# Kernel optimization log

Measured on AMD Instinct MI355X. Metric: run time of the kernel, lower is better.

## Reference

```python
import jax, jax.numpy as jnp
import numpy as np

B, L, H, E = 8, 4096, 8, 64  # in_channels = out_channels = H*E = 512
MODES = 64                   # mode_select_method='else' -> indices = range(MODES)
SCALE = 1.0 / (512 * 512)


def setup_inputs() -> dict:
    key = jax.random.key(0)
    kq, kk, kv, k1, k2 = jax.random.split(key, 5)
    q = jax.random.normal(kq, (B, L, H, E), dtype=jnp.float32)
    k = jax.random.normal(kk, (B, L, H, E), dtype=jnp.float32)
    v = jax.random.normal(kv, (B, L, H, E), dtype=jnp.float32)
    # weights: [num_heads, in_ch//heads, out_ch//heads, modes], scaled randn
    w1 = SCALE * jax.random.normal(k1, (H, E, E, MODES), dtype=jnp.float32)
    w2 = SCALE * jax.random.normal(k2, (H, E, E, MODES), dtype=jnp.float32)
    return {"q": q, "k": k, "v": v, "w1": w1, "w2": w2}


def reference(q, k, v, w1, w2):
    # k, v, mask are unused by FourierBlock.forward
    Bq, Lq, Hq, Eq = q.shape
    modes = w1.shape[-1]
    x = jnp.transpose(q, (0, 2, 3, 1))          # [B, H, E, L]
    x_ft = jnp.fft.rfft(x, axis=-1)             # [B, H, E, L//2+1] complex
    # With mode_select_method='else', selected indices are 0..modes-1.
    W = (w1 + 1j * w2).astype(x_ft.dtype)       # [H, E_in, E_out, modes]
    # Fused gather + batched complex matmul over all modes (replaces the per-mode loop)
    out_ft = jnp.einsum('bhim,hiom->bhom', x_ft[..., :modes], W)  # [B, H, E, modes]
    # irfft with n=L zero-pads the freq axis from `modes` up to L//2+1 (FEDformer quirk)
    x_out = jnp.fft.irfft(out_ft, n=Lq, axis=-1)  # [B, H, E, L] real
    return jnp.transpose(x_out, (0, 3, 1, 2))     # [B, L, H, E]
```

## Files before the change

### kernel.cpp

```cpp
#include <hip/hip_runtime.h>
#include <hip/hip_bf16.h>
#include <math.h>

#define NB 8
#define LN 4096
#define NH 8
#define NE 64
#define NC 512
#define NM 64
#define LMASK 4095

typedef short s16x8 __attribute__((ext_vector_type(8)));
typedef float f32x4 __attribute__((ext_vector_type(4)));
typedef const __attribute__((address_space(1))) void gv_t;
typedef __attribute__((address_space(3))) void lv_t;

#define WS_EGF 0
#define WS_TF  262144
#define WS_GF  524288
#define WS_XP  786432
#define WS_XS  4980736

static __device__ __forceinline__ unsigned short bf16bits(float f) {
    __hip_bfloat16 b = __float2bfloat16(f);
    return *reinterpret_cast<unsigned short*>(&b);
}

__global__ __launch_bounds__(256) void k_tables(unsigned short* __restrict__ egf,
                                                unsigned short* __restrict__ tfp) {
    const int bid = blockIdx.x;
    const int s = (bid & 255) * 256 + threadIdx.x;
    const int lane = s & 63;
    unsigned short v[8];
    if (bid < 256) {
        int mt = (s >> 6) & 7, kc = s >> 9;
        int r = lane & 15, kg = lane >> 4;
        int mpm = mt * 16 + r;
        int m = mpm >> 1, isim = mpm & 1;
        #pragma unroll
        for (int j = 0; j < 8; ++j) {
            int l = kc * 32 + kg * 8 + j;
            int tw = (m * l) & LMASK;
            float ang = (6.283185307179586f / 4096.0f) * (float)tw;
            v[j] = bf16bits(isim ? -sinf(ang) : cosf(ang));
        }
    } else {
        int lt = (s >> 6) & 255, kk = s >> 14;
        int l = lt * 16 + (lane & 15);
        int khi = (lane >> 4) * 8;
        #pragma unroll
        for (int j = 0; j < 8; ++j) {
            int mp = kk * 32 + khi + j;
            int m = mp >> 1;
            int tw = (m * l) & LMASK;
            float ang = (6.283185307179586f / 4096.0f) * (float)tw;
            v[j] = bf16bits((mp & 1) ? sinf(ang) : cosf(ang));
        }
    }
    uint4 pk;
    pk.x = (unsigned)v[0] | ((unsigned)v[1] << 16);
    pk.y = (unsigned)v[2] | ((unsigned)v[3] << 16);
    pk.z = (unsigned)v[4] | ((unsigned)v[5] << 16);
    pk.w = (unsigned)v[6] | ((unsigned)v[7] << 16);
    unsigned short* dst = (bid < 256) ? egf : tfp;
    *reinterpret_cast<uint4*>(dst + (size_t)s * 8) = pk;
}

__global__ __launch_bounds__(256, 2) void k_fs1(const float* __restrict__ q,
                                                const unsigned short* __restrict__ egf,
                                                float* __restrict__ xp) {
    __shared__ float qlds[4][4][32][16];
    __shared__ unsigned short eglds[4][4096];
    const int ks = blockIdx.x, h = blockIdx.y, b = blockIdx.z;
    const int tid = threadIdx.x;
    const int w = tid >> 6, lane = tid & 63;
    const int g = lane >> 4, r = lane & 15;

    const float* qsrc = q + (((size_t)b * LN + ks * 512 + (lane >> 2)) * NH + h) * NE
                          + w * 16 + (lane & 3) * 4;
    const unsigned short* esrc = egf + (size_t)(ks * 16) * 4096 + w * 1024 + lane * 8;

#define STAGE_Q(T) { \
    __builtin_amdgcn_global_load_lds((gv_t*)(qsrc + (size_t)(T) * 32 * NC), \
        (lv_t*)(&qlds[(T) & 3][w][0][0]), 16, 0, 0); \
    __builtin_amdgcn_global_load_lds((gv_t*)(qsrc + ((size_t)(T) * 32 + 16) * NC), \
        (lv_t*)(&qlds[(T) & 3][w][16][0]), 16, 0, 0); }

#define STAGE_E(T) { \
    __builtin_amdgcn_global_load_lds((gv_t*)(esrc + (size_t)(T) * 4096), \
        (lv_t*)(&eglds[(T) & 3][w * 1024]), 16, 0, 0); \
    __builtin_amdgcn_global_load_lds((gv_t*)(esrc + (size_t)(T) * 4096 + 512), \
        (lv_t*)(&eglds[(T) & 3][w * 1024 + 512]), 16, 0, 0); }

    f32x4 acc[8];
    #pragma unroll
    for (int mt = 0; mt < 8; ++mt) acc[mt] = (f32x4)(0.0f);

    STAGE_Q(0) STAGE_E(0) STAGE_E(1) STAGE_Q(1) STAGE_Q(2)

    #pragma unroll
    for (int t = 0; t < 16; ++t) {
        if (t + 2 < 16) STAGE_E(t + 2)
        if (t <= 13)      asm volatile("s_waitcnt vmcnt(8)" ::: "memory");
        else if (t == 14) asm volatile("s_waitcnt vmcnt(4)" ::: "memory");
        else              asm volatile("s_waitcnt vmcnt(0)" ::: "memory");
        __builtin_amdgcn_s_barrier();
        asm volatile("" ::: "memory");
        if (t + 3 < 16) STAGE_Q(t + 3)

        s16x8 af[8];
        #pragma unroll
        for (int mt = 0; mt < 8; ++mt)
            af[mt] = *reinterpret_cast<const s16x8*>(&eglds[t & 3][mt * 512 + lane * 8]);
        s16x8 bfr;
        #pragma unroll
        for (int j = 0; j < 8; ++j)
            bfr[j] = (short)bf16bits(qlds[t & 3][w][g * 8 + j][r]);

        #pragma unroll
        for (int mt = 0; mt < 8; ++mt)
            acc[mt] = __builtin_amdgcn_mfma_f32_16x16x32_bf16(af[mt], bfr, acc[mt], 0, 0, 0);
    }
#undef STAGE_Q
#undef STAGE_E

    const int i = w * 16 + r;
    float* xpb = xp + ((size_t)ks * 64 + b * 8 + h) * (64 * 128) + (size_t)i * 128 + g * 4;
    #pragma unroll
    for (int mt = 0; mt < 8; ++mt)
        *reinterpret_cast<f32x4*>(xpb + mt * 16) = acc[mt];
}

__global__ __launch_bounds__(256) void k_presum(const float* __restrict__ xp,
                                                float* __restrict__ xs) {
    int e4 = blockIdx.x * 256 + threadIdx.x;
    const f32x4* xp4 = reinterpret_cast<const f32x4*>(xp);
    f32x4 s = (f32x4)(0.0f);
    #pragma unroll
    for (int ks = 0; ks < 8; ++ks)
        s += __builtin_nontemporal_load(&xp4[(size_t)ks * 131072 + e4]);
    reinterpret_cast<f32x4*>(xs)[e4] = s;
}

__global__ __launch_bounds__(256) void k_s2(const float* __restrict__ w1,
                                            const float* __restrict__ w2,
                                            const float* __restrict__ xs,
                                            unsigned short* __restrict__ gf) {
    __shared__ float2 sxs[2][64][64];
    const int sid = blockIdx.x;
    const int x   = sid & 7;
    const int idx = sid >> 3;
    const int r   = x * 8 + (idx & 7);
    const int og  = r >> 3, h = r & 7;
    const int bb  = idx >> 3;
    const int tt  = threadIdx.x;

    {
        float4* dst = reinterpret_cast<float4*>(&sxs[0][0][0]);
        #pragma unroll
        for (int bs = 0; bs < 2; ++bs) {
            const float4* s4 = reinterpret_cast<const float4*>(
                xs + ((size_t)((bb * 2 + bs) * 8 + h)) * 8192);
            #pragma unroll
            for (int k = 0; k < 8; ++k)
                dst[bs * 2048 + k * 256 + tt] = s4[k * 256 + tt];
        }
    }
    __syncthreads();

    const int m    = tt & 63;
    const int osub = tt >> 6;
    const int o0   = og * 8 + osub * 2;

    float re[2][2], im[2][2];
    #pragma unroll
    for (int oo = 0; oo < 2; ++oo)
        #pragma unroll
        for (int bs = 0; bs < 2; ++bs) { re[oo][bs] = 0.f; im[oo][bs] = 0.f; }

    const float* w1p = w1 + (size_t)h * (NE * NE * NM) + (size_t)o0 * NM + m;
    const float* w2p = w2 + (size_t)h * (NE * NE * NM) + (size_t)o0 * NM + m;

    #pragma unroll 8
    for (int i = 0; i < NE; ++i) {
        float wr0 = w1p[(size_t)i * (NE * NM)];
        float wi0 = w2p[(size_t)i * (NE * NM)];
        float wr1 = w1p[(size_t)i * (NE * NM) + NM];
        float wi1 = w2p[(size_t)i * (NE * NM) + NM];
        #pragma unroll
        for (int bs = 0; bs < 2; ++bs) {
            float2 xv = sxs[bs][i][m];
            re[0][bs] = fmaf(xv.x, wr0, fmaf(-xv.y, wi0, re[0][bs]));
            im[0][bs] = fmaf(xv.x, wi0, fmaf( xv.y, wr0, im[0][bs]));
            re[1][bs] = fmaf(xv.x, wr1, fmaf(-xv.y, wi1, re[1][bs]));
            im[1][bs] = fmaf(xv.x, wi1, fmaf( xv.y, wr1, im[1][bs]));
        }
    }

    const float sca = (m == 0 ? 1.0f : 2.0f) / (float)LN;
    const int kk  = m >> 4;
    const int khi = ((m & 15) >> 2) * 16;
    const int jj  = (m & 3) << 1;
    #pragma unroll
    for (int oo = 0; oo < 2; ++oo) {
        const int c = h * 64 + o0 + oo;
        #pragma unroll
        for (int bs = 0; bs < 2; ++bs) {
            const int b = bb * 2 + bs;
            size_t slot = (((size_t)b * 4 + kk) * 32 + (c >> 4)) * 64 + khi + (c & 15);
            unsigned int pk = (unsigned)bf16bits(re[oo][bs] * sca) |
                              ((unsigned)bf16bits(-im[oo][bs] * sca) << 16);
            *reinterpret_cast<unsigned int*>(gf + slot * 8 + jj) = pk;
        }
    }
}

__global__ __launch_bounds__(256, 2) void k_s3(const unsigned short* __restrict__ gf,
                                               const unsigned short* __restrict__ tfp,
                                               float* __restrict__ out) {
    const int lb = blockIdx.x;
    const int cb = blockIdx.y;
    const int b  = blockIdx.z;
    const int tid = threadIdx.x;
    const int w = tid >> 6, lane = tid & 63;

    const unsigned short* ga = gf + ((((size_t)b * 4) * 32 + cb * 8 + w * 2) * 64 + lane) * 8;
    const unsigned short* tb = tfp + (((size_t)lb * 4) * 64 + lane) * 8;

    f32x4 acc[2][4] = {};
    s16x8 af[3][2], bf[3][4];

#define S3_LOAD(T, SLOT)                                                          \
    {                                                                             \
        const unsigned short* gp_ = ga + (size_t)(T) * (32 * 64 * 8);             \
        const unsigned short* tp_ = tb + (size_t)(T) * (256 * 64 * 8);            \
        af[SLOT][0] = *reinterpret_cast<const s16x8*>(gp_);                       \
        af[SLOT][1] = *reinterpret_cast<const s16x8*>(gp_ + 64 * 8);              \
        bf[SLOT][0] = *reinterpret_cast<const s16x8*>(tp_);                       \
        bf[SLOT][1] = *reinterpret_cast<const s16x8*>(tp_ + 64 * 8);              \
        bf[SLOT][2] = *reinterpret_cast<const s16x8*>(tp_ + 2 * 64 * 8);          \
        bf[SLOT][3] = *reinterpret_cast<const s16x8*>(tp_ + 3 * 64 * 8);          \
    }

    S3_LOAD(0, 0)
    S3_LOAD(1, 1)

    #pragma unroll
    for (int t = 0; t < 4; ++t) {
        const int slot = t % 3;
        if (t + 2 < 4) { const int ns = (t + 2) % 3; S3_LOAD(t + 2, ns) }
        #pragma unroll
        for (int mi = 0; mi < 2; ++mi)
            #pragma unroll
            for (int ni = 0; ni < 4; ++ni)
                acc[mi][ni] = __builtin_amdgcn_mfma_f32_16x16x32_bf16(
                    af[slot][mi], bf[slot][ni], acc[mi][ni], 0, 0, 0);
    }
#undef S3_LOAD

    const int c0 = cb * 128 + w * 32 + (lane >> 4) * 4;
    const int l0 = lb * 64 + (lane & 15);
    #pragma unroll
    for (int mi = 0; mi < 2; ++mi)
        #pragma unroll
        for (int ni = 0; ni < 4; ++ni) {
            float* op = out + ((size_t)b * LN + l0 + ni * 16) * NC + c0 + mi * 16;
            __builtin_nontemporal_store(acc[mi][ni], reinterpret_cast<f32x4*>(op));
        }
}

extern "C" void kernel_launch(void* const* d_in, const int* in_sizes, int n_in,
                              void* d_out, int out_size, void* d_ws, size_t ws_size,
                              hipStream_t stream) {
    const float* q  = (const float*)d_in[0];
    const float* w1 = (const float*)d_in[3];
    const float* w2 = (const float*)d_in[4];
    float* out = (float*)d_out;
    float* ws  = (float*)d_ws;

    unsigned short* egf = (unsigned short*)(ws + WS_EGF);
    unsigned short* tfp = (unsigned short*)(ws + WS_TF);
    unsigned short* gf  = (unsigned short*)(ws + WS_GF);
    float*          xp  = ws + WS_XP;
    float*          xs  = ws + WS_XS;

    k_tables<<<512, 256, 0, stream>>>(egf, tfp);
    k_fs1<<<dim3(8, NH, NB), 256, 0, stream>>>(q, egf, xp);
    k_presum<<<512, 256, 0, stream>>>(xp, xs);
    k_s2<<<256, 256, 0, stream>>>(w1, w2, xs, gf);
    k_s3<<<dim3(64, 4, NB), 256, 0, stream>>>(gf, tfp, out);
}
```

Measured before the change: 56.99 us.

## Compute forward DFT twiddles inline in k_fs1 and merge inverse table into presum

Drops the separate table-building kernel. k_fs1 now generates its forward DFT twiddle tile in registers with fast __sinf/__cosf, using incremental angle stepping, and writes it to a smaller double-buffered LDS slot instead of staging it from global memory. The inverse twiddle table is built by extra blocks appended to the presum launch. This removes one kernel launch and the global round trip for the forward table, but puts transcendental math inside the MFMA loop and uses lower-accuracy intrinsics.

```diff
diff --git a/kernel.cpp b/kernel.cpp
--- a/kernel.cpp
+++ b/kernel.cpp
@@ -15,7 +15,6 @@
 typedef const __attribute__((address_space(1))) void gv_t;
 typedef __attribute__((address_space(3))) void lv_t;
 
-#define WS_EGF 0
 #define WS_TF  262144
 #define WS_GF  524288
 #define WS_XP  786432
@@ -26,120 +25,122 @@
     return *reinterpret_cast<unsigned short*>(&b);
 }
 
-__global__ __launch_bounds__(256) void k_tables(unsigned short* __restrict__ egf,
+__global__ __launch_bounds__(256, 2) void k_fs1(const float* __restrict__ q,
+                                                float* __restrict__ xp) {
+    __shared__ float qlds[4][4][32][16];
+    __shared__ unsigned short eglds[2][4096];
+    const int ks = blockIdx.x, h = blockIdx.y, b = blockIdx.z;
+    const int tid = threadIdx.x;
+    const int w = tid >> 6, lane = tid & 63;
+    const int g = lane >> 4, r = lane & 15;
+
+    const float* qsrc = q + (((size_t)b * LN + ks * 512 + (lane >> 2)) * NH + h) * NE
+                          + w * 16 + (lane & 3) * 4;
+
+    const int m_tw  = (tid >> 5) * 8 + (tid & 7);
+    const int kg_tw = (tid >> 3) & 3;
+
+#define STAGE_Q(T) { \
+    __builtin_amdgcn_global_load_lds((gv_t*)(qsrc + (size_t)(T) * 32 * NC), \
+        (lv_t*)(&qlds[(T) & 3][w][0][0]), 16, 0, 0); \
+    __builtin_amdgcn_global_load_lds((gv_t*)(qsrc + ((size_t)(T) * 32 + 16) * NC), \
+        (lv_t*)(&qlds[(T) & 3][w][16][0]), 16, 0, 0); }
+
+    f32x4 acc[8];
+    #pragma unroll
+    for (int mt = 0; mt < 8; ++mt) acc[mt] = (f32x4)(0.0f);
+
+    STAGE_Q(0) STAGE_Q(1) STAGE_Q(2)
+
+    #pragma unroll
+    for (int t = 0; t < 16; ++t) {
+        {
+            const int kc = ks * 16 + t;
+            int tw = (m_tw * (kc * 32 + kg_tw * 8)) & LMASK;
+            unsigned short vc[8], vs[8];
+            #pragma unroll
+            for (int j = 0; j < 8; ++j) {
+                float ang = (6.283185307179586f / 4096.0f) * (float)tw;
+                vc[j] = bf16bits(__cosf(ang));
+                vs[j] = bf16bits(-__sinf(ang));
+                tw = (tw + m_tw) & LMASK;
+            }
+            uint4 p0, p1;
+            p0.x = (unsigned)vc[0] | ((unsigned)vc[1] << 16);
+            p0.y = (unsigned)vc[2] | ((unsigned)vc[3] << 16);
+            p0.z = (unsigned)vc[4] | ((unsigned)vc[5] << 16);
+            p0.w = (unsigned)vc[6] | ((unsigned)vc[7] << 16);
+            p1.x = (unsigned)vs[0] | ((unsigned)vs[1] << 16);
+            p1.y = (unsigned)vs[2] | ((unsigned)vs[3] << 16);
+            p1.z = (unsigned)vs[4] | ((unsigned)vs[5] << 16);
+            p1.w = (unsigned)vs[6] | ((unsigned)vs[7] << 16);
+            *reinterpret_cast<uint4*>(&eglds[t & 1][tid * 16])     = p0;
+            *reinterpret_cast<uint4*>(&eglds[t & 1][tid * 16 + 8]) = p1;
+        }
+        if (t <= 13)      asm volatile("s_waitcnt vmcnt(4)" ::: "memory");
+        else if (t == 14) asm volatile("s_waitcnt vmcnt(2)" ::: "memory");
+        else              asm volatile("s_waitcnt vmcnt(0)" ::: "memory");
+        asm volatile("s_waitcnt lgkmcnt(0)" ::: "memory");
+        __builtin_amdgcn_s_barrier();
+        asm volatile("" ::: "memory");
+        if (t + 3 < 16) STAGE_Q(t + 3)
+
+        s16x8 af[8];
+        #pragma unroll
+        for (int mt = 0; mt < 8; ++mt)
+            af[mt] = *reinterpret_cast<const s16x8*>(&eglds[t & 1][mt * 512 + lane * 8]);
+        s16x8 bfr;
+        #pragma unroll
+        for (int j = 0; j < 8; ++j)
+            bfr[j] = (short)bf16bits(qlds[t & 3][w][g * 8 + j][r]);
+
+        #pragma unroll
+        for (int mt = 0; mt < 8; ++mt)
+            acc[mt] = __builtin_amdgcn_mfma_f32_16x16x32_bf16(af[mt], bfr, acc[mt], 0, 0, 0);
+    }
+#undef STAGE_Q
+
+    const int i = w * 16 + r;
+    float* xpb = xp + ((size_t)ks * 64 + b * 8 + h) * (64 * 128) + (size_t)i * 128 + g * 4;
+    #pragma unroll
+    for (int mt = 0; mt < 8; ++mt)
+        *reinterpret_cast<f32x4*>(xpb + mt * 16) = acc[mt];
+}
+
+__global__ __launch_bounds__(256) void k_presum(const float* __restrict__ xp,
+                                                float* __restrict__ xs,
                                                 unsigned short* __restrict__ tfp) {
     const int bid = blockIdx.x;
-    const int s = (bid & 255) * 256 + threadIdx.x;
+    if (bid < 512) {
+        int e4 = bid * 256 + threadIdx.x;
+        const f32x4* xp4 = reinterpret_cast<const f32x4*>(xp);
+        f32x4 s = (f32x4)(0.0f);
+        #pragma unroll
+        for (int ks = 0; ks < 8; ++ks)
+            s += __builtin_nontemporal_load(&xp4[(size_t)ks * 131072 + e4]);
+        reinterpret_cast<f32x4*>(xs)[e4] = s;
+        return;
+    }
+    const int s = (bid - 512) * 256 + threadIdx.x;
     const int lane = s & 63;
+    const int lt = (s >> 6) & 255, kk = s >> 14;
+    const int l = lt * 16 + (lane & 15);
+    const int khi = (lane >> 4) * 8;
     unsigned short v[8];
-    if (bid < 256) {
-        int mt = (s >> 6) & 7, kc = s >> 9;
-        int r = lane & 15, kg = lane >> 4;
-        int mpm = mt * 16 + r;
-        int m = mpm >> 1, isim = mpm & 1;
-        #pragma unroll
-        for (int j = 0; j < 8; ++j) {
-            int l = kc * 32 + kg * 8 + j;
-            int tw = (m * l) & LMASK;
-            float ang = (6.283185307179586f / 4096.0f) * (float)tw;
-            v[j] = bf16bits(isim ? -sinf(ang) : cosf(ang));
-        }
-    } else {
-        int lt = (s >> 6) & 255, kk = s >> 14;
-        int l = lt * 16 + (lane & 15);
-        int khi = (lane >> 4) * 8;
-        #pragma unroll
-        for (int j = 0; j < 8; ++j) {
-            int mp = kk * 32 + khi + j;
-            int m = mp >> 1;
-            int tw = (m * l) & LMASK;
-            float ang = (6.283185307179586f / 4096.0f) * (float)tw;
-            v[j] = bf16bits((mp & 1) ? sinf(ang) : cosf(ang));
-        }
+    #pragma unroll
+    for (int j = 0; j < 8; ++j) {
+        int mp = kk * 32 + khi + j;
+        int m = mp >> 1;
+        int tw = (m * l) & LMASK;
+        float ang = (6.283185307179586f / 4096.0f) * (float)tw;
+        v[j] = bf16bits((mp & 1) ? sinf(ang) : cosf(ang));
     }
     uint4 pk;
     pk.x = (unsigned)v[0] | ((unsigned)v[1] << 16);
     pk.y = (unsigned)v[2] | ((unsigned)v[3] << 16);
     pk.z = (unsigned)v[4] | ((unsigned)v[5] << 16);
     pk.w = (unsigned)v[6] | ((unsigned)v[7] << 16);
-    unsigned short* dst = (bid < 256) ? egf : tfp;
-    *reinterpret_cast<uint4*>(dst + (size_t)s * 8) = pk;
-}
-
-__global__ __launch_bounds__(256, 2) void k_fs1(const float* __restrict__ q,
-                                                const unsigned short* __restrict__ egf,
-                                                float* __restrict__ xp) {
-    __shared__ float qlds[4][4][32][16];
-    __shared__ unsigned short eglds[4][4096];
-    const int ks = blockIdx.x, h = blockIdx.y, b = blockIdx.z;
-    const int tid = threadIdx.x;
-    const int w = tid >> 6, lane = tid & 63;
-    const int g = lane >> 4, r = lane & 15;
-
-    const float* qsrc = q + (((size_t)b * LN + ks * 512 + (lane >> 2)) * NH + h) * NE
-                          + w * 16 + (lane & 3) * 4;
-    const unsigned short* esrc = egf + (size_t)(ks * 16) * 4096 + w * 1024 + lane * 8;
-
-#define STAGE_Q(T) { \
-    __builtin_amdgcn_global_load_lds((gv_t*)(qsrc + (size_t)(T) * 32 * NC), \
-        (lv_t*)(&qlds[(T) & 3][w][0][0]), 16, 0, 0); \
-    __builtin_amdgcn_global_load_lds((gv_t*)(qsrc + ((size_t)(T) * 32 + 16) * NC), \
-        (lv_t*)(&qlds[(T) & 3][w][16][0]), 16, 0, 0); }
-
-#define STAGE_E(T) { \
-    __builtin_amdgcn_global_load_lds((gv_t*)(esrc + (size_t)(T) * 4096), \
-        (lv_t*)(&eglds[(T) & 3][w * 1024]), 16, 0, 0); \
-    __builtin_amdgcn_global_load_lds((gv_t*)(esrc + (size_t)(T) * 4096 + 512), \
-        (lv_t*)(&eglds[(T) & 3][w * 1024 + 512]), 16, 0, 0); }
-
-    f32x4 acc[8];
-    #pragma unroll
-    for (int mt = 0; mt < 8; ++mt) acc[mt] = (f32x4)(0.0f);
-
-    STAGE_Q(0) STAGE_E(0) STAGE_E(1) STAGE_Q(1) STAGE_Q(2)
-
-    #pragma unroll
-    for (int t = 0; t < 16; ++t) {
-        if (t + 2 < 16) STAGE_E(t + 2)
-        if (t <= 13)      asm volatile("s_waitcnt vmcnt(8)" ::: "memory");
-        else if (t == 14) asm volatile("s_waitcnt vmcnt(4)" ::: "memory");
-        else              asm volatile("s_waitcnt vmcnt(0)" ::: "memory");
-        __builtin_amdgcn_s_barrier();
-        asm volatile("" ::: "memory");
-        if (t + 3 < 16) STAGE_Q(t + 3)
-
-        s16x8 af[8];
-        #pragma unroll
-        for (int mt = 0; mt < 8; ++mt)
-            af[mt] = *reinterpret_cast<const s16x8*>(&eglds[t & 3][mt * 512 + lane * 8]);
-        s16x8 bfr;
-        #pragma unroll
-        for (int j = 0; j < 8; ++j)
-            bfr[j] = (short)bf16bits(qlds[t & 3][w][g * 8 + j][r]);
-
-        #pragma unroll
-        for (int mt = 0; mt < 8; ++mt)
-            acc[mt] = __builtin_amdgcn_mfma_f32_16x16x32_bf16(af[mt], bfr, acc[mt], 0, 0, 0);
-    }
-#undef STAGE_Q
-#undef STAGE_E
-
-    const int i = w * 16 + r;
-    float* xpb = xp + ((size_t)ks * 64 + b * 8 + h) * (64 * 128) + (size_t)i * 128 + g * 4;
-    #pragma unroll
-    for (int mt = 0; mt < 8; ++mt)
-        *reinterpret_cast<f32x4*>(xpb + mt * 16) = acc[mt];
-}
-
-__global__ __launch_bounds__(256) void k_presum(const float* __restrict__ xp,
-                                                float* __restrict__ xs) {
-    int e4 = blockIdx.x * 256 + threadIdx.x;
-    const f32x4* xp4 = reinterpret_cast<const f32x4*>(xp);
-    f32x4 s = (f32x4)(0.0f);
-    #pragma unroll
-    for (int ks = 0; ks < 8; ++ks)
-        s += __builtin_nontemporal_load(&xp4[(size_t)ks * 131072 + e4]);
-    reinterpret_cast<f32x4*>(xs)[e4] = s;
+    *reinterpret_cast<uint4*>(tfp + (size_t)s * 8) = pk;
 }
 
 __global__ __launch_bounds__(256) void k_s2(const float* __restrict__ w1,
@@ -278,15 +279,13 @@
     float* out = (float*)d_out;
     float* ws  = (float*)d_ws;
 
-    unsigned short* egf = (unsigned short*)(ws + WS_EGF);
     unsigned short* tfp = (unsigned short*)(ws + WS_TF);
     unsigned short* gf  = (unsigned short*)(ws + WS_GF);
     float*          xp  = ws + WS_XP;
     float*          xs  = ws + WS_XS;
 
-    k_tables<<<512, 256, 0, stream>>>(egf, tfp);
-    k_fs1<<<dim3(8, NH, NB), 256, 0, stream>>>(q, egf, xp);
-    k_presum<<<512, 256, 0, stream>>>(xp, xs);
+    k_fs1<<<dim3(8, NH, NB), 256, 0, stream>>>(q, xp);
+    k_presum<<<768, 256, 0, stream>>>(xp, xs, tfp);
     k_s2<<<256, 256, 0, stream>>>(w1, w2, xs, gf);
     k_s3<<<dim3(64, 4, NB), 256, 0, stream>>>(gf, tfp, out);
 }
```

Measured after the change: 53.90 us. 1.06x faster.
